# Kernel tuning notes

Measured on AMD Instinct MI355X. Metric: run time of the kernel, lower is better.

Reference implementation:

```python
import jax, jax.numpy as jnp
import numpy as np

N = 100000          # nodes
E = 1600000         # edges (avg degree 16)
IN_DIM = 64
HID = 64
OUT = 32
NUM_GRAPHS = 64


def setup_inputs() -> dict:
    key = jax.random.key(0)
    ks = jax.random.split(key, 12)
    x = jax.random.normal(ks[0], (N, IN_DIM), dtype=jnp.float32)
    edge_index = jax.random.randint(ks[1], (2, E), 0, N, dtype=jnp.int64)
    batch = jnp.sort(jax.random.randint(ks[2], (N,), 0, NUM_GRAPHS, dtype=jnp.int64))
    s = 0.05
    return {
        "x": x,
        "edge_index": edge_index,
        "batch": batch,
        "w1_init": jax.random.normal(ks[3], (IN_DIM, HID), dtype=jnp.float32) * s,
        "w1_root": jax.random.normal(ks[4], (IN_DIM, HID), dtype=jnp.float32) * s,
        "b1": jnp.zeros((HID,), dtype=jnp.float32),
        "w2_init": jax.random.normal(ks[5], (HID, HID), dtype=jnp.float32) * s,
        "w2_root": jax.random.normal(ks[6], (HID, HID), dtype=jnp.float32) * s,
        "b2": jnp.zeros((HID,), dtype=jnp.float32),
        "fc_w": jax.random.normal(ks[7], (HID, OUT), dtype=jnp.float32) * s,
        "fc_b": jnp.zeros((OUT,), dtype=jnp.float32),
    }


def reference(x, edge_index, batch, w1_init, w1_root, b1, w2_init, w2_root, b2, fc_w, fc_b):
    row, col = edge_index[0], edge_index[1]
    # gcn_norm without self loops (ARMAConv default): deg over target nodes
    ones_e = jnp.ones((E,), dtype=x.dtype)
    deg = jax.ops.segment_sum(ones_e, col, num_segments=N)
    dinv = jnp.where(deg > 0, jax.lax.rsqrt(jnp.maximum(deg, 1.0)), 0.0)
    norm = dinv[row] * dinv[col]  # [E]

    def propagate(h):  # out[col] += norm * h[row]
        return jax.ops.segment_sum(h[row] * norm[:, None], col, num_segments=N)

    # ARMAConv (K=1, T=1, act=None): A_hat (x W_init) + x W_root + b
    h = jax.nn.relu(propagate(x @ w1_init) + x @ w1_root + b1)
    h = jax.nn.relu(propagate(h @ w2_init) + h @ w2_root + b2)

    # global mean pool over graphs
    cnt = jax.ops.segment_sum(jnp.ones((N,), dtype=h.dtype), batch, num_segments=NUM_GRAPHS)
    pooled = jax.ops.segment_sum(h, batch, num_segments=NUM_GRAPHS) / jnp.maximum(cnt, 1.0)[:, None]

    return pooled @ fc_w + fc_b  # [NUM_GRAPHS, OUT]
```

## Files before the change

kernel.cpp:

```cpp
#include <hip/hip_runtime.h>
#include <hip/hip_bf16.h>


#define NB 256
#define CAP 5120
#define MAXB 400
#define P1_CHUNK 2048

typedef unsigned int uint32;
typedef unsigned short ushort16;
typedef __attribute__((ext_vector_type(8))) short short8;
typedef __attribute__((ext_vector_type(4))) float f32x4;

__device__ inline uint32 bf16rn(float f) {
    uint32 u = __float_as_uint(f);
    uint32 r = ((u >> 16) & 1u) + 0x7FFFu;
    return (u + r) >> 16;
}
__device__ inline uint32 pack_bf16(float a, float b) {
    return bf16rn(a) | (bf16rn(b) << 16);
}

__global__ __launch_bounds__(256) void bucket_kernel(
    const int* __restrict__ row, const int* __restrict__ col,
    uint32* __restrict__ bpack, int* __restrict__ bcnt, int E) {
    __shared__ int hist[MAXB];
    __shared__ int ofs[MAXB];
    __shared__ int cur[MAXB];
    __shared__ int gbase[MAXB];
    __shared__ int s[256];
    __shared__ uint32 stage[P1_CHUNK];
    __shared__ unsigned short stage_bk[P1_CHUNK];

    int t = threadIdx.x;
    for (int i = t; i < MAXB; i += 256) hist[i] = 0;
    __syncthreads();

    int e0 = blockIdx.x * P1_CHUNK;
    int cntE = min(E - e0, P1_CHUNK);

    for (int i = t; i < cntE; i += 256) {
        int c = col[e0 + i];
        atomicAdd(&hist[c >> 8], 1);
    }
    __syncthreads();

    int i2 = 2 * t;
    int a = (i2 < MAXB) ? hist[i2] : 0;
    int b = (i2 + 1 < MAXB) ? hist[i2 + 1] : 0;
    s[t] = a + b;
    __syncthreads();
    for (int off = 1; off < 256; off <<= 1) {
        int x = (t >= off) ? s[t - off] : 0;
        __syncthreads();
        s[t] += x;
        __syncthreads();
    }
    int excl = (t > 0) ? s[t - 1] : 0;
    if (i2 < MAXB) ofs[i2] = excl;
    if (i2 + 1 < MAXB) ofs[i2 + 1] = excl + a;
    __syncthreads();

    for (int i = t; i < MAXB; i += 256) {
        cur[i] = ofs[i];
        gbase[i] = hist[i] ? atomicAdd(&bcnt[i], hist[i]) : 0;
    }
    __syncthreads();

    for (int i = t; i < cntE; i += 256) {
        int c = col[e0 + i];
        int r = row[e0 + i];
        int bk = c >> 8;
        int k = atomicAdd(&cur[bk], 1);
        stage[k] = ((uint32)(c & 255) << 24) | (uint32)r;
        stage_bk[k] = (unsigned short)bk;
    }
    __syncthreads();

    for (int i = t; i < cntE; i += 256) {
        uint32 pk = stage[i];
        int bk = stage_bk[i];
        int gd = gbase[bk] + (i - ofs[bk]);
        if (gd < CAP) bpack[(size_t)bk * CAP + gd] = pk;
    }
}

__global__ __launch_bounds__(1024) void csr_kernel(
    const uint32* __restrict__ bpack, const int* __restrict__ bcnt,
    int* __restrict__ es, int* __restrict__ nstart, int* __restrict__ ndeg,
    float* __restrict__ dinv, int n) {
    __shared__ int h[NB];
    __shared__ int s[NB];
    __shared__ int cur[NB];
    int b = blockIdx.x, t = threadIdx.x;
    if (t < NB) h[t] = 0;
    __syncthreads();
    int cnt = min(bcnt[b], CAP);
    size_t base = (size_t)b * CAP;
    for (int i = t; i < cnt; i += 1024) {
        int cl = (int)(bpack[base + i] >> 24);
        atomicAdd(&h[cl], 1);
    }
    __syncthreads();
    if (t < NB) s[t] = h[t];
    __syncthreads();
    for (int off = 1; off < NB; off <<= 1) {
        int x = 0;
        if (t < NB && t >= off) x = s[t - off];
        __syncthreads();
        if (t < NB) s[t] += x;
        __syncthreads();
    }
    if (t < NB) {
        int myofs = s[t] - h[t];
        cur[t] = myofs;
        int node = b * NB + t;
        if (node < n) {
            nstart[node] = (int)base + myofs;
            ndeg[node] = h[t];
            dinv[node] = h[t] ? rsqrtf((float)h[t]) : 0.0f;
        }
    }
    __syncthreads();
    for (int i = t; i < cnt; i += 1024) {
        uint32 pk = bpack[base + i];
        int cl = (int)(pk >> 24);
        int p = atomicAdd(&cur[cl], 1);
        es[base + p] = (int)(pk & 0xFFFFFFu);
    }
}

__global__ __launch_bounds__(256) void cvt_kernel(
    const float* __restrict__ X, uint32* __restrict__ Xb2, int total4) {
    int i = blockIdx.x * 256 + threadIdx.x;
    if (i < total4) {
        float4 v = *(const float4*)&X[(size_t)i * 4];
        Xb2[(size_t)i * 2]     = pack_bf16(v.x, v.y);
        Xb2[(size_t)i * 2 + 1] = pack_bf16(v.z, v.w);
    }
}

__global__ __launch_bounds__(256) void wprep_kernel(
    const float* __restrict__ W1i, const float* __restrict__ W1r,
    const float* __restrict__ W2i, const float* __restrict__ W2r,
    ushort16* __restrict__ wt) {
    int idx = blockIdx.x * 256 + threadIdx.x;
    if (idx >= 8 * 4096) return;
    int m = idx >> 12;
    int r = idx & 4095;
    int d = r >> 6, k = r & 63;
    const float* W = (m < 2) ? W1i : (m < 4) ? W1r : (m < 6) ? W2i : W2r;
    float v = W[k * 64 + d];
    uint32 hi = bf16rn(v);
    uint32 outv;
    if (m & 1) {
        float hf = __uint_as_float(hi << 16);
        outv = bf16rn(v - hf);
    } else {
        outv = hi;
    }
    wt[(size_t)m * 4096 + d * 64 + k] = (unsigned short)outv;
}

__global__ __launch_bounds__(256) void gemm_mfma(
    const uint32* __restrict__ Xb2,
    const ushort16* __restrict__ wt4,
    const float* __restrict__ bias, const float* __restrict__ dinv,
    ushort16* __restrict__ Ts, ushort16* __restrict__ Rs, int n) {
    __shared__ unsigned short sXs[64 * 72];
    int t = threadIdx.x;
    int node0 = blockIdx.x * 64;

    for (int i = t; i < 512; i += 256) {
        int r = i >> 3, kg = i & 7;
        int node = node0 + r;
        uint4 v = make_uint4(0u, 0u, 0u, 0u);
        if (node < n) v = *(const uint4*)&Xb2[(size_t)node * 32 + kg * 4];
        *(uint4*)&sXs[r * 72 + kg * 8] = v;
    }

    int w = t >> 6;
    int lane = t & 63;
    int q = lane >> 4;
    int col = lane & 15;
    int dim = w * 16 + col;

    short8 bih[2], bil[2], brh[2], brl[2];
#pragma unroll
    for (int kh = 0; kh < 2; ++kh) {
        size_t o = (size_t)dim * 64 + kh * 32 + q * 8;
        bih[kh] = *(const short8*)&wt4[0 * 4096 + o];
        bil[kh] = *(const short8*)&wt4[1 * 4096 + o];
        brh[kh] = *(const short8*)&wt4[2 * 4096 + o];
        brl[kh] = *(const short8*)&wt4[3 * 4096 + o];
    }
    float bi = bias[dim];
    __syncthreads();

#pragma unroll
    for (int mt = 0; mt < 4; ++mt) {
        int rbase = mt * 16 + col;
        short8 a0 = *(const short8*)&sXs[rbase * 72 + q * 8];
        short8 a1 = *(const short8*)&sXs[rbase * 72 + 32 + q * 8];
        f32x4 accT = {0.f, 0.f, 0.f, 0.f};
        f32x4 accR = {0.f, 0.f, 0.f, 0.f};
        accT = __builtin_amdgcn_mfma_f32_16x16x32_bf16(a0, bih[0], accT, 0, 0, 0);
        accT = __builtin_amdgcn_mfma_f32_16x16x32_bf16(a1, bih[1], accT, 0, 0, 0);
        accT = __builtin_amdgcn_mfma_f32_16x16x32_bf16(a0, bil[0], accT, 0, 0, 0);
        accT = __builtin_amdgcn_mfma_f32_16x16x32_bf16(a1, bil[1], accT, 0, 0, 0);
        accR = __builtin_amdgcn_mfma_f32_16x16x32_bf16(a0, brh[0], accR, 0, 0, 0);
        accR = __builtin_amdgcn_mfma_f32_16x16x32_bf16(a1, brh[1], accR, 0, 0, 0);
        accR = __builtin_amdgcn_mfma_f32_16x16x32_bf16(a0, brl[0], accR, 0, 0, 0);
        accR = __builtin_amdgcn_mfma_f32_16x16x32_bf16(a1, brl[1], accR, 0, 0, 0);
#pragma unroll
        for (int reg = 0; reg < 4; ++reg) {
            int node = node0 + mt * 16 + q * 4 + reg;
            if (node < n) {
                float dv = dinv[node];
                Ts[(size_t)node * 64 + dim] = (unsigned short)bf16rn(accT[reg] * dv);
                Rs[(size_t)node * 64 + dim] = (unsigned short)bf16rn(accR[reg] + bi);
            }
        }
    }
}

__global__ __launch_bounds__(256) void gather_fused(
    const uint32* __restrict__ Ts, const uint32* __restrict__ Rs,
    const int* __restrict__ es, const int* __restrict__ nstart,
    const int* __restrict__ ndeg, const float* __restrict__ dinv,
    uint32* __restrict__ Hb, int n) {
    int c = blockIdx.x * 4 + (threadIdx.x >> 6);
    if (c >= n) return;
    int lane = threadIdx.x & 63;
    int half = lane >> 5;
    int d2 = lane & 31;
    int deg = ndeg[c];
    int s0 = nstart[c];
    float a0 = 0.0f, a1 = 0.0f;
    for (int base = 0; base < deg; base += 64) {
        int m = min(deg - base, 64);
        int sid = (lane < m) ? es[s0 + base + lane] : 0;
        int j = 0;
        for (; j + 16 <= m; j += 16) {
            int r0 = __shfl(sid, j + half);
            int r1 = __shfl(sid, j + 2 + half);
            int r2 = __shfl(sid, j + 4 + half);
            int r3 = __shfl(sid, j + 6 + half);
            int r4 = __shfl(sid, j + 8 + half);
            int r5 = __shfl(sid, j + 10 + half);
            int r6 = __shfl(sid, j + 12 + half);
            int r7 = __shfl(sid, j + 14 + half);
            uint32 u0 = Ts[(size_t)r0 * 32 + d2];
            uint32 u1 = Ts[(size_t)r1 * 32 + d2];
            uint32 u2 = Ts[(size_t)r2 * 32 + d2];
            uint32 u3 = Ts[(size_t)r3 * 32 + d2];
            uint32 u4 = Ts[(size_t)r4 * 32 + d2];
            uint32 u5 = Ts[(size_t)r5 * 32 + d2];
            uint32 u6 = Ts[(size_t)r6 * 32 + d2];
            uint32 u7 = Ts[(size_t)r7 * 32 + d2];
            a0 += __uint_as_float(u0 << 16) + __uint_as_float(u1 << 16)
                + __uint_as_float(u2 << 16) + __uint_as_float(u3 << 16)
                + __uint_as_float(u4 << 16) + __uint_as_float(u5 << 16)
                + __uint_as_float(u6 << 16) + __uint_as_float(u7 << 16);
            a1 += __uint_as_float(u0 & 0xFFFF0000u) + __uint_as_float(u1 & 0xFFFF0000u)
                + __uint_as_float(u2 & 0xFFFF0000u) + __uint_as_float(u3 & 0xFFFF0000u)
                + __uint_as_float(u4 & 0xFFFF0000u) + __uint_as_float(u5 & 0xFFFF0000u)
                + __uint_as_float(u6 & 0xFFFF0000u) + __uint_as_float(u7 & 0xFFFF0000u);
        }
        for (; j + 8 <= m; j += 8) {
            int r0 = __shfl(sid, j + half);
            int r1 = __shfl(sid, j + 2 + half);
            int r2 = __shfl(sid, j + 4 + half);
            int r3 = __shfl(sid, j + 6 + half);
            uint32 u0 = Ts[(size_t)r0 * 32 + d2];
            uint32 u1 = Ts[(size_t)r1 * 32 + d2];
            uint32 u2 = Ts[(size_t)r2 * 32 + d2];
            uint32 u3 = Ts[(size_t)r3 * 32 + d2];
            a0 += __uint_as_float(u0 << 16) + __uint_as_float(u1 << 16)
                + __uint_as_float(u2 << 16) + __uint_as_float(u3 << 16);
            a1 += __uint_as_float(u0 & 0xFFFF0000u) + __uint_as_float(u1 & 0xFFFF0000u)
                + __uint_as_float(u2 & 0xFFFF0000u) + __uint_as_float(u3 & 0xFFFF0000u);
        }
        for (; j < m; j += 2) {
            int e = j + half;
            int rr = __shfl(sid, (e < m) ? e : 0);
            if (e < m) {
                uint32 u = Ts[(size_t)rr * 32 + d2];
                a0 += __uint_as_float(u << 16);
                a1 += __uint_as_float(u & 0xFFFF0000u);
            }
        }
    }
    a0 += __shfl_xor(a0, 32);
    a1 += __shfl_xor(a1, 32);
    if (half == 0) {
        float dc = dinv[c];
        uint32 ur = Rs[(size_t)c * 32 + d2];
        float rv0 = __uint_as_float(ur << 16);
        float rv1 = __uint_as_float(ur & 0xFFFF0000u);
        float h0 = fmaxf(fmaf(dc, a0, rv0), 0.0f);
        float h1 = fmaxf(fmaf(dc, a1, rv1), 0.0f);
        Hb[(size_t)c * 32 + d2] = pack_bf16(h0, h1);
    }
}

__global__ __launch_bounds__(256) void pool_kernel(
    const ushort16* __restrict__ Hin, const int* __restrict__ batch,
    float* __restrict__ pooled, float* __restrict__ cnt, int n) {
    __shared__ float sAcc[64 * 64];
    __shared__ float sCnt[64];
    int tid = threadIdx.x;
    for (int i = tid; i < 4096; i += 256) sAcc[i] = 0.0f;
    if (tid < 64) sCnt[tid] = 0.0f;
    __syncthreads();

    int w = tid >> 6, d = tid & 63;
    int s = blockIdx.x * 256 + w * 64;
    int e = min(s + 64, n);
    float acc = 0.0f, c = 0.0f;
    int gcur = -1;
    for (int i = s; i < e; ++i) {
        int g = batch[i];
        if (g != gcur) {
            if (gcur >= 0) {
                atomicAdd(&sAcc[gcur * 64 + d], acc);
                if (d == 0) atomicAdd(&sCnt[gcur], c);
            }
            gcur = g; acc = 0.0f; c = 0.0f;
        }
        acc += __uint_as_float(((uint32)Hin[(size_t)i * 64 + d]) << 16);
        c += 1.0f;
    }
    if (gcur >= 0) {
        atomicAdd(&sAcc[gcur * 64 + d], acc);
        if (d == 0) atomicAdd(&sCnt[gcur], c);
    }
    __syncthreads();
    for (int i = tid; i < 4096; i += 256) {
        float v = sAcc[i];
        if (v != 0.0f) atomicAdd(&pooled[i], v);
    }
    if (tid < 64) {
        float v = sCnt[tid];
        if (v != 0.0f) atomicAdd(&cnt[tid], v);
    }
}

__global__ void final_fc(const float* __restrict__ pooled, const float* __restrict__ cnt,
                         const float* __restrict__ fcw, const float* __restrict__ fcb,
                         float* __restrict__ out) {
    int idx = blockIdx.x * 256 + threadIdx.x;
    if (idx >= 64 * 32) return;
    int g = idx >> 5, o = idx & 31;
    float c = fmaxf(cnt[g], 1.0f);
    float acc = 0.0f;
#pragma unroll
    for (int k = 0; k < 64; ++k) acc = fmaf(pooled[g * 64 + k], fcw[k * 32 + o], acc);
    out[idx] = acc / c + fcb[o];
}

extern "C" void kernel_launch(void* const* d_in, const int* in_sizes, int n_in,
                              void* d_out, int out_size, void* d_ws, size_t ws_size,
                              hipStream_t stream) {
    const float* x       = (const float*)d_in[0];
    const int*   eidx    = (const int*)d_in[1];
    const int*   batch   = (const int*)d_in[2];
    const float* w1_init = (const float*)d_in[3];
    const float* w1_root = (const float*)d_in[4];
    const float* b1      = (const float*)d_in[5];
    const float* w2_init = (const float*)d_in[6];
    const float* w2_root = (const float*)d_in[7];
    const float* b2      = (const float*)d_in[8];
    const float* fc_w    = (const float*)d_in[9];
    const float* fc_b    = (const float*)d_in[10];
    float* out = (float*)d_out;

    const int N = in_sizes[0] / 64;
    const int E = in_sizes[1] / 2;
    const int* row = eidx;
    const int* col = eidx + E;

    const int B = (N + NB - 1) / NB;

    uint32* bpack = (uint32*)d_ws;
    int*   es     = (int*)(bpack + (size_t)B * CAP);
    int*   bcnt   = es + (size_t)B * CAP;
    float* pooled = (float*)(bcnt + MAXB);
    float* cnt    = pooled + 64 * 64;
    int*   nstart = (int*)(cnt + 64);
    int*   ndeg   = nstart + N;
    float* dinv   = (float*)(ndeg + N);
    uint32* wtU   = (uint32*)(dinv + N);
    uint32* Xb    = wtU + 16384;
    uint32* Ts    = Xb + (size_t)N * 32;
    uint32* Rs    = Ts + (size_t)N * 32;
    uint32* Hb    = Rs + (size_t)N * 32;
    ushort16* wt  = (ushort16*)wtU;

    hipMemsetAsync(bcnt, 0, (size_t)(MAXB + 64 * 64 + 64) * sizeof(int), stream);

    bucket_kernel<<<(E + P1_CHUNK - 1) / P1_CHUNK, 256, 0, stream>>>(row, col, bpack, bcnt, E);
    csr_kernel<<<B, 1024, 0, stream>>>(bpack, bcnt, es, nstart, ndeg, dinv, N);
    cvt_kernel<<<(N * 16 + 255) / 256, 256, 0, stream>>>(x, Xb, N * 16);
    wprep_kernel<<<(8 * 4096 + 255) / 256, 256, 0, stream>>>(w1_init, w1_root, w2_init, w2_root, wt);

    gemm_mfma<<<(N + 63) / 64, 256, 0, stream>>>(Xb, wt, b1, dinv,
                                                 (ushort16*)Ts, (ushort16*)Rs, N);
    gather_fused<<<(N + 3) / 4, 256, 0, stream>>>(Ts, Rs, es, nstart, ndeg, dinv, Hb, N);

    gemm_mfma<<<(N + 63) / 64, 256, 0, stream>>>(Hb, wt + (size_t)4 * 4096, b2, dinv,
                                                 (ushort16*)Ts, (ushort16*)Rs, N);
    gather_fused<<<(N + 3) / 4, 256, 0, stream>>>(Ts, Rs, es, nstart, ndeg, dinv, Hb, N);

    pool_kernel<<<(N + 255) / 256, 256, 0, stream>>>((const ushort16*)Hb, batch, pooled, cnt, N);
    final_fc<<<(64 * 32 + 255) / 256, 256, 0, stream>>>(pooled, cnt, fc_w, fc_b, out);
}
```

Before: 314.9 us.

## Fuse input conversion and weight prep into GEMM, cache CSR buckets in LDS

Drops the separate fp32→bf16 conversion and weight-split kernels. The first GEMM now reads fp32 x directly and converts while staging it into shared memory, and every GEMM block builds its own hi/lo bf16 weight fragments from the fp32 weights. The CSR build keeps the bucket words in shared memory instead of reading them from global memory twice. The pool kernel is rewritten to read packed bf16 pairs per lane with two node streams per wave. This saves two launches and an intermediate buffer, but each GEMM block now issues redundant strided weight loads and conversions.

```diff
diff --git a/kernel.cpp b/kernel.cpp
--- a/kernel.cpp
+++ b/kernel.cpp
@@ -89,6 +89,7 @@
     const uint32* __restrict__ bpack, const int* __restrict__ bcnt,
     int* __restrict__ es, int* __restrict__ nstart, int* __restrict__ ndeg,
     float* __restrict__ dinv, int n) {
+    __shared__ uint32 sbp[CAP];
     __shared__ int h[NB];
     __shared__ int s[NB];
     __shared__ int cur[NB];
@@ -98,8 +99,9 @@
     int cnt = min(bcnt[b], CAP);
     size_t base = (size_t)b * CAP;
     for (int i = t; i < cnt; i += 1024) {
-        int cl = (int)(bpack[base + i] >> 24);
-        atomicAdd(&h[cl], 1);
+        uint32 pk = bpack[base + i];
+        sbp[i] = pk;
+        atomicAdd(&h[pk >> 24], 1);
     }
     __syncthreads();
     if (t < NB) s[t] = h[t];
@@ -123,60 +125,43 @@
     }
     __syncthreads();
     for (int i = t; i < cnt; i += 1024) {
-        uint32 pk = bpack[base + i];
+        uint32 pk = sbp[i];
         int cl = (int)(pk >> 24);
         int p = atomicAdd(&cur[cl], 1);
         es[base + p] = (int)(pk & 0xFFFFFFu);
     }
 }
 
-__global__ __launch_bounds__(256) void cvt_kernel(
-    const float* __restrict__ X, uint32* __restrict__ Xb2, int total4) {
-    int i = blockIdx.x * 256 + threadIdx.x;
-    if (i < total4) {
-        float4 v = *(const float4*)&X[(size_t)i * 4];
-        Xb2[(size_t)i * 2]     = pack_bf16(v.x, v.y);
-        Xb2[(size_t)i * 2 + 1] = pack_bf16(v.z, v.w);
-    }
-}
-
-__global__ __launch_bounds__(256) void wprep_kernel(
-    const float* __restrict__ W1i, const float* __restrict__ W1r,
-    const float* __restrict__ W2i, const float* __restrict__ W2r,
-    ushort16* __restrict__ wt) {
-    int idx = blockIdx.x * 256 + threadIdx.x;
-    if (idx >= 8 * 4096) return;
-    int m = idx >> 12;
-    int r = idx & 4095;
-    int d = r >> 6, k = r & 63;
-    const float* W = (m < 2) ? W1i : (m < 4) ? W1r : (m < 6) ? W2i : W2r;
-    float v = W[k * 64 + d];
-    uint32 hi = bf16rn(v);
-    uint32 outv;
-    if (m & 1) {
-        float hf = __uint_as_float(hi << 16);
-        outv = bf16rn(v - hf);
-    } else {
-        outv = hi;
-    }
-    wt[(size_t)m * 4096 + d * 64 + k] = (unsigned short)outv;
-}
-
 __global__ __launch_bounds__(256) void gemm_mfma(
-    const uint32* __restrict__ Xb2,
-    const ushort16* __restrict__ wt4,
+    const void* __restrict__ Xin,
+    const float* __restrict__ Wi, const float* __restrict__ Wr,
     const float* __restrict__ bias, const float* __restrict__ dinv,
-    ushort16* __restrict__ Ts, ushort16* __restrict__ Rs, int n) {
+    ushort16* __restrict__ Ts, ushort16* __restrict__ Rs, int n, int xf32) {
     __shared__ unsigned short sXs[64 * 72];
     int t = threadIdx.x;
     int node0 = blockIdx.x * 64;
 
-    for (int i = t; i < 512; i += 256) {
-        int r = i >> 3, kg = i & 7;
-        int node = node0 + r;
-        uint4 v = make_uint4(0u, 0u, 0u, 0u);
-        if (node < n) v = *(const uint4*)&Xb2[(size_t)node * 32 + kg * 4];
-        *(uint4*)&sXs[r * 72 + kg * 8] = v;
+    if (xf32) {
+        const float* X = (const float*)Xin;
+        for (int i = t; i < 1024; i += 256) {
+            int r = i >> 4, c4 = (i & 15) * 4;
+            int node = node0 + r;
+            float4 v = make_float4(0.f, 0.f, 0.f, 0.f);
+            if (node < n) v = *(const float4*)&X[(size_t)node * 64 + c4];
+            uint32 p0 = pack_bf16(v.x, v.y);
+            uint32 p1 = pack_bf16(v.z, v.w);
+            *(uint32*)&sXs[r * 72 + c4] = p0;
+            *(uint32*)&sXs[r * 72 + c4 + 2] = p1;
+        }
+    } else {
+        const uint32* Xb2 = (const uint32*)Xin;
+        for (int i = t; i < 512; i += 256) {
+            int r = i >> 3, kg = i & 7;
+            int node = node0 + r;
+            uint4 v = make_uint4(0u, 0u, 0u, 0u);
+            if (node < n) v = *(const uint4*)&Xb2[(size_t)node * 32 + kg * 4];
+            *(uint4*)&sXs[r * 72 + kg * 8] = v;
+        }
     }
 
     int w = t >> 6;
@@ -188,11 +173,20 @@
     short8 bih[2], bil[2], brh[2], brl[2];
 #pragma unroll
     for (int kh = 0; kh < 2; ++kh) {
-        size_t o = (size_t)dim * 64 + kh * 32 + q * 8;
-        bih[kh] = *(const short8*)&wt4[0 * 4096 + o];
-        bil[kh] = *(const short8*)&wt4[1 * 4096 + o];
-        brh[kh] = *(const short8*)&wt4[2 * 4096 + o];
-        brl[kh] = *(const short8*)&wt4[3 * 4096 + o];
+#pragma unroll
+        for (int j = 0; j < 8; ++j) {
+            int k = kh * 32 + q * 8 + j;
+            float vi = Wi[k * 64 + dim];
+            uint32 hi = bf16rn(vi);
+            uint32 lo = bf16rn(vi - __uint_as_float(hi << 16));
+            bih[kh][j] = (short)hi;
+            bil[kh][j] = (short)lo;
+            float vr = Wr[k * 64 + dim];
+            uint32 hr = bf16rn(vr);
+            uint32 lr = bf16rn(vr - __uint_as_float(hr << 16));
+            brh[kh][j] = (short)hr;
+            brl[kh][j] = (short)lr;
+        }
     }
     float bi = bias[dim];
     __syncthreads();
@@ -305,7 +299,7 @@
 }
 
 __global__ __launch_bounds__(256) void pool_kernel(
-    const ushort16* __restrict__ Hin, const int* __restrict__ batch,
+    const uint32* __restrict__ Hb, const int* __restrict__ batch,
     float* __restrict__ pooled, float* __restrict__ cnt, int n) {
     __shared__ float sAcc[64 * 64];
     __shared__ float sCnt[64];
@@ -314,26 +308,31 @@
     if (tid < 64) sCnt[tid] = 0.0f;
     __syncthreads();
 
-    int w = tid >> 6, d = tid & 63;
+    int w = tid >> 6, lane = tid & 63;
+    int half = lane >> 5, d2 = lane & 31;
     int s = blockIdx.x * 256 + w * 64;
     int e = min(s + 64, n);
-    float acc = 0.0f, c = 0.0f;
+    float a0 = 0.0f, a1 = 0.0f, c = 0.0f;
     int gcur = -1;
-    for (int i = s; i < e; ++i) {
+    for (int i = s + half; i < e; i += 2) {
         int g = batch[i];
         if (g != gcur) {
             if (gcur >= 0) {
-                atomicAdd(&sAcc[gcur * 64 + d], acc);
-                if (d == 0) atomicAdd(&sCnt[gcur], c);
+                atomicAdd(&sAcc[gcur * 64 + 2 * d2], a0);
+                atomicAdd(&sAcc[gcur * 64 + 2 * d2 + 1], a1);
+                if (d2 == 0) atomicAdd(&sCnt[gcur], c);
             }
-            gcur = g; acc = 0.0f; c = 0.0f;
-        }
-        acc += __uint_as_float(((uint32)Hin[(size_t)i * 64 + d]) << 16);
+            gcur = g; a0 = 0.0f; a1 = 0.0f; c = 0.0f;
+        }
+        uint32 u = Hb[(size_t)i * 32 + d2];
+        a0 += __uint_as_float(u << 16);
+        a1 += __uint_as_float(u & 0xFFFF0000u);
         c += 1.0f;
     }
     if (gcur >= 0) {
-        atomicAdd(&sAcc[gcur * 64 + d], acc);
-        if (d == 0) atomicAdd(&sCnt[gcur], c);
+        atomicAdd(&sAcc[gcur * 64 + 2 * d2], a0);
+        atomicAdd(&sAcc[gcur * 64 + 2 * d2 + 1], a1);
+        if (d2 == 0) atomicAdd(&sCnt[gcur], c);
     }
     __syncthreads();
     for (int i = tid; i < 4096; i += 256) {
@@ -390,28 +389,23 @@
     int*   nstart = (int*)(cnt + 64);
     int*   ndeg   = nstart + N;
     float* dinv   = (float*)(ndeg + N);
-    uint32* wtU   = (uint32*)(dinv + N);
-    uint32* Xb    = wtU + 16384;
-    uint32* Ts    = Xb + (size_t)N * 32;
+    uint32* Ts    = (uint32*)(dinv + N);
     uint32* Rs    = Ts + (size_t)N * 32;
     uint32* Hb    = Rs + (size_t)N * 32;
-    ushort16* wt  = (ushort16*)wtU;
 
     hipMemsetAsync(bcnt, 0, (size_t)(MAXB + 64 * 64 + 64) * sizeof(int), stream);
 
     bucket_kernel<<<(E + P1_CHUNK - 1) / P1_CHUNK, 256, 0, stream>>>(row, col, bpack, bcnt, E);
     csr_kernel<<<B, 1024, 0, stream>>>(bpack, bcnt, es, nstart, ndeg, dinv, N);
-    cvt_kernel<<<(N * 16 + 255) / 256, 256, 0, stream>>>(x, Xb, N * 16);
-    wprep_kernel<<<(8 * 4096 + 255) / 256, 256, 0, stream>>>(w1_init, w1_root, w2_init, w2_root, wt);
-
-    gemm_mfma<<<(N + 63) / 64, 256, 0, stream>>>(Xb, wt, b1, dinv,
-                                                 (ushort16*)Ts, (ushort16*)Rs, N);
+
+    gemm_mfma<<<(N + 63) / 64, 256, 0, stream>>>(x, w1_init, w1_root, b1, dinv,
+                                                 (ushort16*)Ts, (ushort16*)Rs, N, 1);
     gather_fused<<<(N + 3) / 4, 256, 0, stream>>>(Ts, Rs, es, nstart, ndeg, dinv, Hb, N);
 
-    gemm_mfma<<<(N + 63) / 64, 256, 0, stream>>>(Hb, wt + (size_t)4 * 4096, b2, dinv,
-                                                 (ushort16*)Ts, (ushort16*)Rs, N);
+    gemm_mfma<<<(N + 63) / 64, 256, 0, stream>>>(Hb, w2_init, w2_root, b2, dinv,
+                                                 (ushort16*)Ts, (ushort16*)Rs, N, 0);
     gather_fused<<<(N + 3) / 4, 256, 0, stream>>>(Ts, Rs, es, nstart, ndeg, dinv, Hb, N);
 
-    pool_kernel<<<(N + 255) / 256, 256, 0, stream>>>((const ushort16*)Hb, batch, pooled, cnt, N);
+    pool_kernel<<<(N + 255) / 256, 256, 0, stream>>>(Hb, batch, pooled, cnt, N);
     final_fc<<<(64 * 32 + 255) / 256, 256, 0, stream>>>(pooled, cnt, fc_w, fc_b, out);
 }
```

Measured after the change: 299.7 us. 1.05x faster.
